# Kernel tuning notes

Hardware: AMD Instinct MI355X
Metric: run time of the kernel (lower is better)

## Reference

```python
import jax, jax.numpy as jnp
import numpy as np

B, S, D, H = 4, 2048, 1024, 16
DH = D // H  # 64
EPS = 1e-5


def setup_inputs() -> dict:
    key = jax.random.key(0)
    ks = jax.random.split(key, 6)
    scale = 0.02
    return {
        "x": jax.random.normal(ks[0], (B, S, D), dtype=jnp.float32),
        "Wq": jax.random.normal(ks[1], (H, D, DH), dtype=jnp.float32) * scale,
        "Wk": jax.random.normal(ks[2], (H, D, DH), dtype=jnp.float32) * scale,
        "Wv": jax.random.normal(ks[3], (H, D, DH), dtype=jnp.float32) * scale,
        "Wo": jax.random.normal(ks[4], (D, D), dtype=jnp.float32) * scale,
        "bo": jnp.zeros((D,), dtype=jnp.float32),
        "gamma": jnp.ones((D,), dtype=jnp.float32),
        "beta": jnp.zeros((D,), dtype=jnp.float32),
    }


def reference(x, Wq, Wk, Wv, Wo, bo, gamma, beta):
    # Per-head projections, stacked across heads: [B,H,S,DH]
    q = jnp.einsum("bsd,hdk->bhsk", x, Wq)
    k = jnp.einsum("bsd,hdk->bhsk", x, Wk)
    v = jnp.einsum("bsd,hdk->bhsk", x, Wv)
    inv_scale = 1.0 / jnp.sqrt(jnp.float32(DH))  # key.size(-1) == head_dim
    scores = jnp.einsum("bhqk,bhsk->bhqs", q, k) * inv_scale  # [B,H,S,S]
    attn = jax.nn.softmax(scores, axis=-1)
    ctx = jnp.einsum("bhqs,bhsk->bhqk", attn, v)  # [B,H,S,DH]
    # concat heads -> [B,S,D]
    concat = jnp.transpose(ctx, (0, 2, 1, 3)).reshape(B, S, D)
    proj = concat @ Wo + bo  # fc_out (Wo stored as [in,out])
    added = proj + x  # residual add
    mu = jnp.mean(added, axis=-1, keepdims=True)
    var = jnp.mean(jnp.square(added - mu), axis=-1, keepdims=True)
    normed = (added - mu) * jax.lax.rsqrt(var + EPS)
    return normed * gamma + beta
```

## Files before the change

### kernel.cpp

```cpp
#include <hip/hip_runtime.h>
#include <hip/hip_bf16.h>
#include <stdint.h>

#define DEV __device__ __forceinline__

typedef short s16x8 __attribute__((ext_vector_type(8)));
typedef float f32x4 __attribute__((ext_vector_type(4)));
typedef int i32x4 __attribute__((ext_vector_type(4)));

DEV void async_load16(const void* g, void* l) {
  __builtin_amdgcn_global_load_lds((void __attribute__((address_space(1)))*)(g),
                                   (void __attribute__((address_space(3)))*)(l),
                                   16, 0, 0);
}

DEV unsigned pack_bf16x2(float a, float b) {
  __hip_bfloat162 h = __float22bfloat162_rn(make_float2(a, b));
  union { __hip_bfloat162 h2; unsigned u; } cv;
  cv.h2 = h;
  return cv.u;
}

__global__ __launch_bounds__(256) void cast_x_kernel(const float* __restrict__ in,
                                                     __hip_bfloat16* __restrict__ out, int n4) {
  int i = blockIdx.x * 256 + threadIdx.x;
  if (i >= n4) return;
  float4 v = ((const float4*)in)[i];
  alignas(8) __hip_bfloat16 t[4] = {__float2bfloat16(v.x), __float2bfloat16(v.y),
                                    __float2bfloat16(v.z), __float2bfloat16(v.w)};
  *(uint2*)(out + (size_t)i * 4) = *(const uint2*)t;
}

__global__ __launch_bounds__(256) void transpose_cast_kernel(const float* __restrict__ src,
                                                             __hip_bfloat16* __restrict__ dst,
                                                             int R, int C, float scale) {
  __shared__ float tile[64][65];
  const int r0 = blockIdx.x * 64, c0 = blockIdx.y * 64, bt = blockIdx.z;
  const int tc = threadIdx.x & 63, tr = threadIdx.x >> 6;
  const float* sp = src + (size_t)bt * R * C;
#pragma unroll
  for (int rr = 0; rr < 64; rr += 4)
    tile[tr + rr][tc] = sp[(size_t)(r0 + tr + rr) * C + c0 + tc];
  __syncthreads();
  __hip_bfloat16* dp = dst + (size_t)bt * R * C;
#pragma unroll
  for (int rr = 0; rr < 64; rr += 4) {
    int cc = tr + rr;
    dp[(size_t)(c0 + cc) * R + r0 + tc] = __float2bfloat16(tile[tc][cc] * scale);
  }
}

template <int MODE>
__global__ __launch_bounds__(256) void gemm128(const __hip_bfloat16* __restrict__ A,
                                               const __hip_bfloat16* __restrict__ Bt,
                                               void* __restrict__ out0,
                                               void* __restrict__ out1,
                                               void* __restrict__ out2,
                                               const float* __restrict__ bias,
                                               const float* __restrict__ resid,
                                               int M, int N, int K) {
  __shared__ __hip_bfloat16 As[128 * 32];
  __shared__ __hip_bfloat16 Bs[128 * 32];
  const int tid = threadIdx.x;
  const int lane = tid & 63, w = tid >> 6;
  const int lr = lane & 15, lq = lane >> 4;
  const int wm = w >> 1, wn = w & 1;
  const int m0 = blockIdx.y * 128, n0 = blockIdx.x * 128;

  const f32x4 fz = {0.f, 0.f, 0.f, 0.f};
  f32x4 acc[4][4];
#pragma unroll
  for (int i = 0; i < 4; i++)
#pragma unroll
    for (int j = 0; j < 4; j++) acc[i][j] = fz;

  const int kiters = K >> 5;
  for (int kt = 0; kt < kiters; kt++) {
    __syncthreads();
#pragma unroll
    for (int r = 0; r < 2; r++) {
      const int c = r * 256 + tid;
      const int row = c >> 2, kc = c & 3;
      async_load16((const short*)A + (size_t)(m0 + row) * K + kt * 32 + kc * 8,
                   (char*)As + (r * 256 + (tid & 0xC0)) * 16);
      async_load16((const short*)Bt + (size_t)(n0 + row) * K + kt * 32 + kc * 8,
                   (char*)Bs + (r * 256 + (tid & 0xC0)) * 16);
    }
    __syncthreads();
    const short* Ap = (const short*)As;
    const short* Bp = (const short*)Bs;
    s16x8 av[4], bv[4];
#pragma unroll
    for (int i = 0; i < 4; i++)
      av[i] = *(const s16x8*)(Ap + (wm * 64 + i * 16 + lr) * 32 + lq * 8);
#pragma unroll
    for (int j = 0; j < 4; j++)
      bv[j] = *(const s16x8*)(Bp + (wn * 64 + j * 16 + lr) * 32 + lq * 8);
#pragma unroll
    for (int i = 0; i < 4; i++)
#pragma unroll
      for (int j = 0; j < 4; j++)
        acc[i][j] = __builtin_amdgcn_mfma_f32_16x16x32_bf16(av[i], bv[j], acc[i][j], 0, 0, 0);
  }

  if constexpr (MODE == 0) {
    if (n0 < 2048) {
      __hip_bfloat16* dst01 = (__hip_bfloat16*)((n0 < 1024) ? out0 : out1);
#pragma unroll
      for (int i = 0; i < 4; i++)
#pragma unroll
        for (int j = 0; j < 4; j++)
#pragma unroll
          for (int r = 0; r < 4; r++) {
            const int row = m0 + wm * 64 + i * 16 + lq * 4 + r;
            const int col = n0 + wn * 64 + j * 16 + lr;
            const int bb = row >> 11, s = row & 2047;
            const int colq = col & 1023;
            dst01[((((size_t)bb * 16 + (colq >> 6)) * 2048 + s) << 6) + (col & 63)] =
                __float2bfloat16(acc[i][j][r]);
          }
    } else {
#pragma unroll
      for (int i = 0; i < 4; i++)
#pragma unroll
        for (int j = 0; j < 4; j++) {
          const int row0 = m0 + wm * 64 + i * 16 + lq * 4;
          const int col = (n0 - 2048) + wn * 64 + j * 16 + lr;
          const int bb = row0 >> 11, s0 = row0 & 2047;
          alignas(8) __hip_bfloat16 t4[4] = {
              __float2bfloat16(acc[i][j][0]), __float2bfloat16(acc[i][j][1]),
              __float2bfloat16(acc[i][j][2]), __float2bfloat16(acc[i][j][3])};
          *(uint2*)((__hip_bfloat16*)out2 + (size_t)bb * 2097152 + (size_t)col * 2048 + s0) =
              *(const uint2*)t4;
        }
    }
  } else {
#pragma unroll
    for (int i = 0; i < 4; i++)
#pragma unroll
      for (int j = 0; j < 4; j++)
#pragma unroll
        for (int r = 0; r < 4; r++) {
          const int row = m0 + wm * 64 + i * 16 + lq * 4 + r;
          const int col = n0 + wn * 64 + j * 16 + lr;
          const size_t idx = (size_t)row * 1024 + col;
          ((float*)out0)[idx] = acc[i][j][r] + bias[col] + resid[idx];
        }
  }
}

__global__ __launch_bounds__(256, 3) void flash_kernel(const __hip_bfloat16* __restrict__ Qg,
                                                       const __hip_bfloat16* __restrict__ Kg,
                                                       const __hip_bfloat16* __restrict__ Vtg,
                                                       __hip_bfloat16* __restrict__ Og) {
  __shared__ alignas(16) char smem[33792];
  __hip_bfloat16* Klds = (__hip_bfloat16*)smem;
  __hip_bfloat16* Vlds = (__hip_bfloat16*)(smem + 16384);
  float* xch = (float*)smem;
  float* lx = (float*)(smem + 32768);
  const int tid = threadIdx.x;
  const int lane = tid & 63, w = tid >> 6;
  const int lr = lane & 15, lq = lane >> 4;
  const int hb = blockIdx.x, qt = blockIdx.y;
  const int h = hb >> 2, b = hb & 3;
  const size_t bh = (size_t)b * 16 + h;
  const short* Qbase = (const short*)Qg + (bh * 2048 + (size_t)qt * 64) * 64;
  const short* Kbh = (const short*)Kg + bh * 2048 * 64;
  const short* Vbh = (const short*)Vtg + bh * 64 * 2048;

  const int rbase = (lr >> 2) * 8 + (lr & 3);
  const int gk = (lr & 3) | (((lr >> 2) & 1) << 2);

  s16x8 qb[4][2];
#pragma unroll
  for (int nt = 0; nt < 4; nt++)
#pragma unroll
    for (int ks = 0; ks < 2; ks++)
      qb[nt][ks] = *(const s16x8*)(Qbase + (nt * 16 + lr) * 64 + ks * 32 + lq * 8);

  const f32x4 fz = {0.f, 0.f, 0.f, 0.f};
  f32x4 o[4][4];
#pragma unroll
  for (int i = 0; i < 4; i++)
#pragma unroll
    for (int j = 0; j < 4; j++) o[i][j] = fz;
  float lsum[4] = {0.f, 0.f, 0.f, 0.f};

  for (int kb = 0; kb < 16; kb++) {
    __syncthreads();
    const short* Ksrc = Kbh + kb * 128 * 64;
#pragma unroll
    for (int r = 0; r < 4; r++) {
      int c = r * 256 + tid;
      int row = c >> 3, ck = c & 7;
      int g = (row & 3) | (((row >> 3) & 1) << 2);
      async_load16(Ksrc + row * 64 + (ck ^ g) * 8,
                   (char*)Klds + (r * 256 + (tid & 0xC0)) * 16);
    }
#pragma unroll
    for (int r = 0; r < 4; r++) {
      int c = r * 256 + tid;
      int row = c >> 4, ck = c & 15;
      async_load16(Vbh + (size_t)row * 2048 + kb * 128 + (ck ^ (row & 15)) * 8,
                   (char*)Vlds + (r * 256 + (tid & 0xC0)) * 16);
    }
    __syncthreads();

    const short* Kp = (const short*)Klds;
    const short* Vp = (const short*)Vlds;

    union { i32x4 i; s16x8 s; } pa[4];
#pragma unroll
    for (int mt = 0; mt < 2; mt++) {
      const int kvrow = w * 32 + mt * 4 + rbase;
      s16x8 kf0 = *(const s16x8*)(Kp + kvrow * 64 + ((0 * 4 + lq) ^ gk) * 8);
      s16x8 kf1 = *(const s16x8*)(Kp + kvrow * 64 + ((1 * 4 + lq) ^ gk) * 8);
#pragma unroll
      for (int nt = 0; nt < 4; nt++) {
        f32x4 st = fz;
        st = __builtin_amdgcn_mfma_f32_16x16x32_bf16(kf0, qb[nt][0], st, 0, 0, 0);
        st = __builtin_amdgcn_mfma_f32_16x16x32_bf16(kf1, qb[nt][1], st, 0, 0, 0);
        float e0 = __builtin_amdgcn_exp2f(st[0]);
        float e1 = __builtin_amdgcn_exp2f(st[1]);
        float e2 = __builtin_amdgcn_exp2f(st[2]);
        float e3 = __builtin_amdgcn_exp2f(st[3]);
        lsum[nt] += (e0 + e1) + (e2 + e3);
        pa[nt].i[mt * 2 + 0] = (int)pack_bf16x2(e0, e1);
        pa[nt].i[mt * 2 + 1] = (int)pack_bf16x2(e2, e3);
      }
    }
#pragma unroll
    for (int ndh = 0; ndh < 4; ndh++) {
      int vrow = ndh * 16 + lr;
      s16x8 vb = *(const s16x8*)(Vp + vrow * 128 + (((w * 4 + lq) ^ lr) << 3));
#pragma unroll
      for (int nt = 0; nt < 4; nt++)
        o[nt][ndh] = __builtin_amdgcn_mfma_f32_16x16x32_bf16(pa[nt].s, vb, o[nt][ndh], 0, 0, 0);
    }
  }

#pragma unroll
  for (int nt = 0; nt < 4; nt++) {
    lsum[nt] += __shfl_xor(lsum[nt], 16);
    lsum[nt] += __shfl_xor(lsum[nt], 32);
  }

  __syncthreads();
  if (w >= 2) {
    float* dst = xch + (w - 2) * 4096;
#pragma unroll
    for (int nt = 0; nt < 4; nt++)
#pragma unroll
      for (int ndh = 0; ndh < 4; ndh++)
#pragma unroll
        for (int r = 0; r < 4; r++)
          dst[(nt * 16 + lq * 4 + r) * 64 + ndh * 16 + lr] = o[nt][ndh][r];
  }
  if (lq == 0) {
#pragma unroll
    for (int nt = 0; nt < 4; nt++) lx[w * 64 + nt * 16 + lr] = lsum[nt];
  }
  __syncthreads();
  if (w < 2) {
    const float* src = xch + w * 4096;
#pragma unroll
    for (int nt = 0; nt < 4; nt++) {
#pragma unroll
      for (int ndh = 0; ndh < 4; ndh++)
#pragma unroll
        for (int r = 0; r < 4; r++)
          o[nt][ndh][r] += src[(nt * 16 + lq * 4 + r) * 64 + ndh * 16 + lr];
      lsum[nt] += lx[(w + 2) * 64 + nt * 16 + lr];
    }
  }
  __syncthreads();
  if (w == 1) {
#pragma unroll
    for (int nt = 0; nt < 4; nt++)
#pragma unroll
      for (int ndh = 0; ndh < 4; ndh++)
#pragma unroll
        for (int r = 0; r < 4; r++)
          xch[(nt * 16 + lq * 4 + r) * 64 + ndh * 16 + lr] = o[nt][ndh][r];
    if (lq == 0) {
#pragma unroll
      for (int nt = 0; nt < 4; nt++) lx[64 + nt * 16 + lr] = lsum[nt];
    }
  }
  __syncthreads();
  if (w == 0) {
#pragma unroll
    for (int nt = 0; nt < 4; nt++) {
#pragma unroll
      for (int ndh = 0; ndh < 4; ndh++)
#pragma unroll
        for (int r = 0; r < 4; r++)
          o[nt][ndh][r] += xch[(nt * 16 + lq * 4 + r) * 64 + ndh * 16 + lr];
      lsum[nt] += lx[64 + nt * 16 + lr];
    }
#pragma unroll
    for (int nt = 0; nt < 4; nt++)
#pragma unroll
      for (int r = 0; r < 4; r++) {
        float lv = __shfl(lsum[nt], lq * 4 + r);
        float inv = __builtin_amdgcn_rcpf(lv);
        int rowg = qt * 64 + nt * 16 + lq * 4 + r;
#pragma unroll
        for (int ndh = 0; ndh < 4; ndh++) {
          Og[((size_t)b * 2048 + rowg) * 1024 + h * 64 + ndh * 16 + lr] =
              __float2bfloat16(o[nt][ndh][r] * inv);
        }
      }
  }
}

__global__ __launch_bounds__(256) void ln_kernel(const float* __restrict__ tmp,
                                                 const float* __restrict__ gamma,
                                                 const float* __restrict__ beta,
                                                 float* __restrict__ out) {
  const int row = blockIdx.x, tid = threadIdx.x;
  const int lane = tid & 63, w = tid >> 6;
  const float* rp = tmp + (size_t)row * 1024;
  float4 v = ((const float4*)rp)[tid];
  float s = v.x + v.y + v.z + v.w;
  float ss = v.x * v.x + v.y * v.y + v.z * v.z + v.w * v.w;
#pragma unroll
  for (int off = 32; off >= 1; off >>= 1) {
    s += __shfl_xor(s, off);
    ss += __shfl_xor(ss, off);
  }
  __shared__ float red[8];
  if (lane == 0) {
    red[w] = s;
    red[4 + w] = ss;
  }
  __syncthreads();
  s = red[0] + red[1] + red[2] + red[3];
  ss = red[4] + red[5] + red[6] + red[7];
  const float mu = s * (1.0f / 1024.0f);
  const float var = ss * (1.0f / 1024.0f) - mu * mu;
  const float rstd = rsqrtf(var + 1e-5f);
  float4 g = ((const float4*)gamma)[tid];
  float4 be = ((const float4*)beta)[tid];
  float4 ov;
  ov.x = (v.x - mu) * rstd * g.x + be.x;
  ov.y = (v.y - mu) * rstd * g.y + be.y;
  ov.z = (v.z - mu) * rstd * g.z + be.z;
  ov.w = (v.w - mu) * rstd * g.w + be.w;
  ((float4*)(out + (size_t)row * 1024))[tid] = ov;
}

extern "C" void kernel_launch(void* const* d_in, const int* in_sizes, int n_in,
                              void* d_out, int out_size, void* d_ws, size_t ws_size,
                              hipStream_t stream) {
  (void)in_sizes; (void)n_in; (void)out_size; (void)ws_size;
  const float* x = (const float*)d_in[0];
  const float* Wq = (const float*)d_in[1];
  const float* Wk = (const float*)d_in[2];
  const float* Wv = (const float*)d_in[3];
  const float* Wo = (const float*)d_in[4];
  const float* bo = (const float*)d_in[5];
  const float* gamma = (const float*)d_in[6];
  const float* beta = (const float*)d_in[7];
  float* out = (float*)d_out;
  char* ws = (char*)d_ws;

  __hip_bfloat16* xb = (__hip_bfloat16*)(ws + 0);
  __hip_bfloat16* wqT = (__hip_bfloat16*)(ws + 16777216);
  __hip_bfloat16* wkT = (__hip_bfloat16*)(ws + 18874368);
  __hip_bfloat16* wvT = (__hip_bfloat16*)(ws + 20971520);
  __hip_bfloat16* woT = (__hip_bfloat16*)(ws + 23068672);
  __hip_bfloat16* Q = (__hip_bfloat16*)(ws + 25165824);
  __hip_bfloat16* Kt = (__hip_bfloat16*)(ws + 41943040);
  __hip_bfloat16* Vt = (__hip_bfloat16*)(ws + 58720256);
  __hip_bfloat16* cc = (__hip_bfloat16*)(ws + 75497472);
  float* tmp = (float*)(ws + 25165824);

  cast_x_kernel<<<8192, 256, 0, stream>>>(x, xb, 2097152);
  transpose_cast_kernel<<<dim3(16, 1, 16), 256, 0, stream>>>(Wq, wqT, 1024, 64,
                                                             0.125f * 1.44269504088896f);
  transpose_cast_kernel<<<dim3(16, 1, 16), 256, 0, stream>>>(Wk, wkT, 1024, 64, 1.0f);
  transpose_cast_kernel<<<dim3(16, 1, 16), 256, 0, stream>>>(Wv, wvT, 1024, 64, 1.0f);
  transpose_cast_kernel<<<dim3(16, 16, 1), 256, 0, stream>>>(Wo, woT, 1024, 1024, 1.0f);

  gemm128<0><<<dim3(24, 64), 256, 0, stream>>>(xb, wqT, Q, Kt, Vt, nullptr, nullptr,
                                               8192, 3072, 1024);

  flash_kernel<<<dim3(64, 32), 256, 0, stream>>>(Q, Kt, Vt, cc);

  gemm128<2><<<dim3(8, 64), 256, 0, stream>>>(cc, woT, tmp, nullptr, nullptr, bo, x,
                                              8192, 1024, 1024);
  ln_kernel<<<8192, 256, 0, stream>>>(tmp, gamma, beta, out);
}
```

Measured before the change: 320.3 us.

## Halve flash-attention workgroup to two waves and merge QKV weight transposes

```diff
diff --git a/kernel.cpp b/kernel.cpp
--- a/kernel.cpp
+++ b/kernel.cpp
@@ -47,6 +47,30 @@
   for (int rr = 0; rr < 64; rr += 4) {
     int cc = tr + rr;
     dp[(size_t)(c0 + cc) * R + r0 + tc] = __float2bfloat16(tile[tc][cc] * scale);
+  }
+}
+
+__global__ __launch_bounds__(256) void qkv_transpose_kernel(const float* __restrict__ Wq,
+                                                            const float* __restrict__ Wk,
+                                                            const float* __restrict__ Wv,
+                                                            __hip_bfloat16* __restrict__ dst,
+                                                            float qscale) {
+  __shared__ float tile[64][65];
+  const int z = blockIdx.z, which = z >> 4, bt = z & 15;
+  const int r0 = blockIdx.x * 64;
+  const int tc = threadIdx.x & 63, tr = threadIdx.x >> 6;
+  const float* src = (which == 0) ? Wq : (which == 1) ? Wk : Wv;
+  const float scale = (which == 0) ? qscale : 1.0f;
+  const float* sp = src + (size_t)bt * 1024 * 64;
+#pragma unroll
+  for (int rr = 0; rr < 64; rr += 4)
+    tile[tr + rr][tc] = sp[(size_t)(r0 + tr + rr) * 64 + tc];
+  __syncthreads();
+  __hip_bfloat16* dp = dst + (size_t)z * 1024 * 64;
+#pragma unroll
+  for (int rr = 0; rr < 64; rr += 4) {
+    int cc = tr + rr;
+    dp[(size_t)(cc)*1024 + r0 + tc] = __float2bfloat16(tile[tc][cc] * scale);
   }
 }
 
@@ -149,15 +173,15 @@
   }
 }
 
-__global__ __launch_bounds__(256, 3) void flash_kernel(const __hip_bfloat16* __restrict__ Qg,
+__global__ __launch_bounds__(128, 3) void flash_kernel(const __hip_bfloat16* __restrict__ Qg,
                                                        const __hip_bfloat16* __restrict__ Kg,
                                                        const __hip_bfloat16* __restrict__ Vtg,
                                                        __hip_bfloat16* __restrict__ Og) {
-  __shared__ alignas(16) char smem[33792];
+  __shared__ alignas(16) char smem[16896];
   __hip_bfloat16* Klds = (__hip_bfloat16*)smem;
-  __hip_bfloat16* Vlds = (__hip_bfloat16*)(smem + 16384);
+  __hip_bfloat16* Vlds = (__hip_bfloat16*)(smem + 8192);
   float* xch = (float*)smem;
-  float* lx = (float*)(smem + 32768);
+  float* lx = (float*)(smem + 16384);
   const int tid = threadIdx.x;
   const int lane = tid & 63, w = tid >> 6;
   const int lr = lane & 15, lq = lane >> 4;
@@ -169,7 +193,7 @@
   const short* Vbh = (const short*)Vtg + bh * 64 * 2048;
 
   const int rbase = (lr >> 2) * 8 + (lr & 3);
-  const int gk = (lr & 3) | (((lr >> 2) & 1) << 2);
+  const int gk = lr & 7;
 
   s16x8 qb[4][2];
 #pragma unroll
@@ -186,23 +210,23 @@
     for (int j = 0; j < 4; j++) o[i][j] = fz;
   float lsum[4] = {0.f, 0.f, 0.f, 0.f};
 
-  for (int kb = 0; kb < 16; kb++) {
+  for (int kb = 0; kb < 32; kb++) {
     __syncthreads();
-    const short* Ksrc = Kbh + kb * 128 * 64;
+    const short* Ksrc = Kbh + kb * 64 * 64;
 #pragma unroll
     for (int r = 0; r < 4; r++) {
-      int c = r * 256 + tid;
+      int c = r * 128 + tid;
       int row = c >> 3, ck = c & 7;
       int g = (row & 3) | (((row >> 3) & 1) << 2);
       async_load16(Ksrc + row * 64 + (ck ^ g) * 8,
-                   (char*)Klds + (r * 256 + (tid & 0xC0)) * 16);
+                   (char*)Klds + (r * 128 + (tid & 64)) * 16);
     }
 #pragma unroll
     for (int r = 0; r < 4; r++) {
-      int c = r * 256 + tid;
-      int row = c >> 4, ck = c & 15;
-      async_load16(Vbh + (size_t)row * 2048 + kb * 128 + (ck ^ (row & 15)) * 8,
-                   (char*)Vlds + (r * 256 + (tid & 0xC0)) * 16);
+      int c = r * 128 + tid;
+      int row = c >> 3, ck = c & 7;
+      async_load16(Vbh + (size_t)row * 2048 + kb * 64 + ((ck ^ (row & 7))) * 8,
+                   (char*)Vlds + (r * 128 + (tid & 64)) * 16);
     }
     __syncthreads();
 
@@ -213,8 +237,8 @@
 #pragma unroll
     for (int mt = 0; mt < 2; mt++) {
       const int kvrow = w * 32 + mt * 4 + rbase;
-      s16x8 kf0 = *(const s16x8*)(Kp + kvrow * 64 + ((0 * 4 + lq) ^ gk) * 8);
-      s16x8 kf1 = *(const s16x8*)(Kp + kvrow * 64 + ((1 * 4 + lq) ^ gk) * 8);
+      s16x8 kf0 = *(const s16x8*)(Kp + kvrow * 64 + (((0 * 4 + lq) ^ gk)) * 8);
+      s16x8 kf1 = *(const s16x8*)(Kp + kvrow * 64 + (((1 * 4 + lq) ^ gk)) * 8);
 #pragma unroll
       for (int nt = 0; nt < 4; nt++) {
         f32x4 st = fz;
@@ -232,7 +256,7 @@
 #pragma unroll
     for (int ndh = 0; ndh < 4; ndh++) {
       int vrow = ndh * 16 + lr;
-      s16x8 vb = *(const s16x8*)(Vp + vrow * 128 + (((w * 4 + lq) ^ lr) << 3));
+      s16x8 vb = *(const s16x8*)(Vp + vrow * 64 + (((w * 4 + lq) ^ (vrow & 7))) * 8);
 #pragma unroll
       for (int nt = 0; nt < 4; nt++)
         o[nt][ndh] = __builtin_amdgcn_mfma_f32_16x16x32_bf16(pa[nt].s, vb, o[nt][ndh], 0, 0, 0);
@@ -246,71 +270,40 @@
   }
 
   __syncthreads();
-  if (w >= 2) {
-    float* dst = xch + (w - 2) * 4096;
-#pragma unroll
-    for (int nt = 0; nt < 4; nt++)
-#pragma unroll
-      for (int ndh = 0; ndh < 4; ndh++)
-#pragma unroll
-        for (int r = 0; r < 4; r++)
-          dst[(nt * 16 + lq * 4 + r) * 64 + ndh * 16 + lr] = o[nt][ndh][r];
-  }
-  if (lq == 0) {
-#pragma unroll
-    for (int nt = 0; nt < 4; nt++) lx[w * 64 + nt * 16 + lr] = lsum[nt];
-  }
-  __syncthreads();
-  if (w < 2) {
-    const float* src = xch + w * 4096;
-#pragma unroll
-    for (int nt = 0; nt < 4; nt++) {
-#pragma unroll
-      for (int ndh = 0; ndh < 4; ndh++)
-#pragma unroll
-        for (int r = 0; r < 4; r++)
-          o[nt][ndh][r] += src[(nt * 16 + lq * 4 + r) * 64 + ndh * 16 + lr];
-      lsum[nt] += lx[(w + 2) * 64 + nt * 16 + lr];
-    }
-  }
-  __syncthreads();
-  if (w == 1) {
-#pragma unroll
-    for (int nt = 0; nt < 4; nt++)
-#pragma unroll
-      for (int ndh = 0; ndh < 4; ndh++)
-#pragma unroll
-        for (int r = 0; r < 4; r++)
-          xch[(nt * 16 + lq * 4 + r) * 64 + ndh * 16 + lr] = o[nt][ndh][r];
-    if (lq == 0) {
-#pragma unroll
-      for (int nt = 0; nt < 4; nt++) lx[64 + nt * 16 + lr] = lsum[nt];
-    }
-  }
-  __syncthreads();
-  if (w == 0) {
-#pragma unroll
-    for (int nt = 0; nt < 4; nt++) {
-#pragma unroll
-      for (int ndh = 0; ndh < 4; ndh++)
-#pragma unroll
-        for (int r = 0; r < 4; r++)
-          o[nt][ndh][r] += xch[(nt * 16 + lq * 4 + r) * 64 + ndh * 16 + lr];
-      lsum[nt] += lx[64 + nt * 16 + lr];
-    }
-#pragma unroll
-    for (int nt = 0; nt < 4; nt++)
-#pragma unroll
-      for (int r = 0; r < 4; r++) {
-        float lv = __shfl(lsum[nt], lq * 4 + r);
-        float inv = __builtin_amdgcn_rcpf(lv);
-        int rowg = qt * 64 + nt * 16 + lq * 4 + r;
-#pragma unroll
-        for (int ndh = 0; ndh < 4; ndh++) {
-          Og[((size_t)b * 2048 + rowg) * 1024 + h * 64 + ndh * 16 + lr] =
-              __float2bfloat16(o[nt][ndh][r] * inv);
-        }
+#pragma unroll
+  for (int ntr = 0; ntr < 2; ntr++) {
+    const int nt_write = 2 * (1 - w) + ntr;
+#pragma unroll
+    for (int ndh = 0; ndh < 4; ndh++)
+      *(f32x4*)(xch + w * 2048 + (ntr * 4 + ndh) * 256 + lane * 4) = o[nt_write][ndh];
+    if (lq == 0) lx[w * 32 + ntr * 16 + lr] = lsum[nt_write];
+  }
+  __syncthreads();
+#pragma unroll
+  for (int ntr = 0; ntr < 2; ntr++) {
+    const int nt = 2 * w + ntr;
+#pragma unroll
+    for (int ndh = 0; ndh < 4; ndh++) {
+      f32x4 add = *(const f32x4*)(xch + (1 - w) * 2048 + (ntr * 4 + ndh) * 256 + lane * 4);
+      o[nt][ndh] += add;
+    }
+    lsum[nt] += lx[(1 - w) * 32 + ntr * 16 + lr];
+  }
+
+#pragma unroll
+  for (int ntr = 0; ntr < 2; ntr++) {
+    const int nt = 2 * w + ntr;
+#pragma unroll
+    for (int r = 0; r < 4; r++) {
+      float lv = __shfl(lsum[nt], lq * 4 + r);
+      float inv = __builtin_amdgcn_rcpf(lv);
+      int rowg = qt * 64 + nt * 16 + lq * 4 + r;
+#pragma unroll
+      for (int ndh = 0; ndh < 4; ndh++) {
+        Og[((size_t)b * 2048 + rowg) * 1024 + h * 64 + ndh * 16 + lr] =
+            __float2bfloat16(o[nt][ndh][r] * inv);
       }
+    }
   }
 }
 
@@ -366,9 +359,7 @@
   char* ws = (char*)d_ws;
 
   __hip_bfloat16* xb = (__hip_bfloat16*)(ws + 0);
-  __hip_bfloat16* wqT = (__hip_bfloat16*)(ws + 16777216);
-  __hip_bfloat16* wkT = (__hip_bfloat16*)(ws + 18874368);
-  __hip_bfloat16* wvT = (__hip_bfloat16*)(ws + 20971520);
+  __hip_bfloat16* wqkvT = (__hip_bfloat16*)(ws + 16777216);
   __hip_bfloat16* woT = (__hip_bfloat16*)(ws + 23068672);
   __hip_bfloat16* Q = (__hip_bfloat16*)(ws + 25165824);
   __hip_bfloat16* Kt = (__hip_bfloat16*)(ws + 41943040);
@@ -377,16 +368,14 @@
   float* tmp = (float*)(ws + 25165824);
 
   cast_x_kernel<<<8192, 256, 0, stream>>>(x, xb, 2097152);
-  transpose_cast_kernel<<<dim3(16, 1, 16), 256, 0, stream>>>(Wq, wqT, 1024, 64,
-                                                             0.125f * 1.44269504088896f);
-  transpose_cast_kernel<<<dim3(16, 1, 16), 256, 0, stream>>>(Wk, wkT, 1024, 64, 1.0f);
-  transpose_cast_kernel<<<dim3(16, 1, 16), 256, 0, stream>>>(Wv, wvT, 1024, 64, 1.0f);
+  qkv_transpose_kernel<<<dim3(16, 1, 48), 256, 0, stream>>>(Wq, Wk, Wv, wqkvT,
+                                                            0.125f * 1.44269504088896f);
   transpose_cast_kernel<<<dim3(16, 16, 1), 256, 0, stream>>>(Wo, woT, 1024, 1024, 1.0f);
 
-  gemm128<0><<<dim3(24, 64), 256, 0, stream>>>(xb, wqT, Q, Kt, Vt, nullptr, nullptr,
+  gemm128<0><<<dim3(24, 64), 256, 0, stream>>>(xb, wqkvT, Q, Kt, Vt, nullptr, nullptr,
                                                8192, 3072, 1024);
 
-  flash_kernel<<<dim3(64, 32), 256, 0, stream>>>(Q, Kt, Vt, cc);
+  flash_kernel<<<dim3(64, 32), 128, 0, stream>>>(Q, Kt, Vt, cc);
 
   gemm128<2><<<dim3(8, 64), 256, 0, stream>>>(cc, woT, tmp, nullptr, nullptr, bo, x,
                                               8192, 1024, 1024);
```

Result: slower. 914.1 us (+185.4%).
